# Kernel tuning notes

Hardware: AMD Instinct MI355X
Metric: run time of the kernel (lower is better)

Reference implementation:

```python
import jax, jax.numpy as jnp
import numpy as np

B, F_IN, N, S = 2, 128, 192, 192   # batch, in_features, n_nodes, seq (seq==n_nodes required by mask broadcast)
H, D = 4, 64                        # n_heads, n_hidden (out_features = H*D = 256)
NEG_SLOPE = 0.2


def setup_inputs() -> dict:
    key = jax.random.key(0)
    ks = jax.random.split(key, 6)
    X = jax.random.normal(ks[0], (B, F_IN, N, S), dtype=jnp.float32)
    A = jax.random.randint(ks[1], (N, N, 1), 0, 2, dtype=jnp.int32)
    W_lin = jax.random.normal(ks[2], (F_IN, H * D), dtype=jnp.float32) * 0.05
    b_lin = jax.random.uniform(ks[3], (H * D,), dtype=jnp.float32)
    W_attn = jax.random.normal(ks[4], (2 * D,), dtype=jnp.float32) * 0.05
    b_attn = jax.random.uniform(ks[5], (1,), dtype=jnp.float32)
    return {"X": X, "A": A, "W_lin": W_lin, "b_lin": b_lin,
            "W_attn": W_attn, "b_attn": b_attn}


def reference(X, A, W_lin, b_lin, W_attn, b_attn):
    # Dropout is identity (eval mode).
    b, f, n, s = X.shape
    x = jnp.transpose(X, (0, 3, 2, 1))                      # (b, s, n, f)
    g = (x @ W_lin + b_lin).reshape(b, s, n, H, D)          # (b, s, n, H, D)
    # attn is affine: attn(cat[g_i, g_j]) = a_src.g_i + a_dst.g_j + b_attn
    a_src, a_dst = W_attn[:D], W_attn[D:]
    s_src = jnp.einsum('bsnhd,d->bsnh', g, a_src)
    s_dst = jnp.einsum('bsnhd,d->bsnh', g, a_dst)
    e = s_src[:, :, :, None, :] + s_dst[:, :, None, :, :] + b_attn[0]  # (b, s, n_i, n_j, H)
    e = jnp.where(e >= 0, e, NEG_SLOPE * e)                 # LeakyReLU
    # torch masked_fill broadcast: mask (n,n,1,1) aligns with e dims (s, n_i, n_j, H)
    e = jnp.where(A[..., None] == 0, -jnp.inf, e)
    alphas = jax.nn.softmax(e, axis=1)                      # softmax over seq dim (dim=1, as in source)
    alphas = jnp.nan_to_num(alphas, nan=0.0)
    # einsum 'mnojh,klphf->mnohf': independent sums over j (alphas) and k,l,p (g)
    sum_g = g.sum(axis=(0, 1, 2))                           # (H, D)
    attn_res = alphas.sum(axis=3)[..., None] * sum_g        # (b, s, n, H, D)
    out = attn_res.reshape(b, s, n, H * D)                  # concat=True
    return jnp.transpose(out, (0, 3, 2, 1))                 # (b, out_features, n, s)
```

## Files before the change

### kernel.cpp

```cpp
#include <hip/hip_runtime.h>
#include <math.h>

#define B_ 2
#define F_ 128
#define N_ 192
#define S_ 192
#define NS_ (N_ * S_)
#define SLOPE 0.2f
#define LOG2E 1.4426950408889634f
#define NEG_INF (-__builtin_inff())

#if defined(__has_builtin)
#if __has_builtin(__builtin_amdgcn_exp2f)
#define EXP2(x) __builtin_amdgcn_exp2f(x)
#else
#define EXP2(x) exp2f(x)
#endif
#else
#define EXP2(x) exp2f(x)
#endif

__device__ __forceinline__ float lrelu(float e) { return fmaxf(e, SLOPE * e); }

#define OFF_WSRC 0
#define OFF_WDST 512
#define OFF_CSRC 1024
#define OFF_CDST 1028
#define OFF_SUMG 1040
#define OFF_PART 1296
#define OFF_SRC  2320
#define OFF_DST2 (OFF_SRC + 8 * NS_)
#define OFF_DST1 (OFF_DST2 + 8 * NS_)
#define OFF_ALPHA (OFF_DST1 + 8 * NS_)

__global__ __launch_bounds__(256) void kPre(const float* __restrict__ X,
                                            const float* __restrict__ W_lin,
                                            const float* __restrict__ b_lin,
                                            const float* __restrict__ W_attn,
                                            const float* __restrict__ b_attn,
                                            float* __restrict__ ws) {
    int blk = blockIdx.x, t = threadIdx.x;
    if (blk < 1024) {
        int sq = blk & 3, f = (blk >> 2) & 127, b = blk >> 9;
        const float4* p = (const float4*)(X + ((size_t)(b * F_ + f)) * NS_ + sq * 9216);
        float acc = 0.f;
#pragma unroll
        for (int k = 0; k < 9; k++) {
            float4 v = p[t + k * 256];
            acc += (v.x + v.y) + (v.z + v.w);
        }
        for (int o = 32; o; o >>= 1) acc += __shfl_down(acc, o, 64);
        __shared__ float red[4];
        if ((t & 63) == 0) red[t >> 6] = acc;
        __syncthreads();
        if (t == 0)
            ws[OFF_PART + sq * 256 + b * 128 + f] = (red[0] + red[1]) + (red[2] + red[3]);
    } else if (blk == 1024) {
        const float4* wa = (const float4*)W_attn;
        for (int c = t; c < 512; c += 256) {
            int f = c >> 2, h = c & 3;
            const float4* wl = (const float4*)(W_lin + f * 256 + h * 64);
            float as = 0.f, ad = 0.f;
#pragma unroll
            for (int q = 0; q < 16; q++) {
                float4 w = wl[q], a1 = wa[q], a2 = wa[16 + q];
                as += w.x * a1.x + w.y * a1.y + w.z * a1.z + w.w * a1.w;
                ad += w.x * a2.x + w.y * a2.y + w.z * a2.z + w.w * a2.w;
            }
            ws[OFF_WSRC + c] = as * LOG2E;
            ws[OFF_WDST + c] = ad * LOG2E;
        }
    } else {
        if (t < 4) {
            float c = 0.f;
            for (int d = 0; d < 64; d++) c += b_lin[t * 64 + d] * W_attn[d];
            ws[OFF_CSRC + t] = (c + b_attn[0]) * LOG2E;
        } else if (t < 8) {
            int h = t - 4;
            float c = 0.f;
            for (int d = 0; d < 64; d++) c += b_lin[h * 64 + d] * W_attn[64 + d];
            ws[OFF_CDST + h] = c * LOG2E;
        }
    }
}

__global__ __launch_bounds__(256) void kProj(const float* __restrict__ X,
                                             const int* __restrict__ A,
                                             const float* __restrict__ W_lin,
                                             const float* __restrict__ b_lin,
                                             float* __restrict__ ws) {
    __shared__ float4 wsl[128], wdl[128];
    __shared__ float red[4 * 64 * 9];
    __shared__ float xs[128];
    __shared__ float wbuf[4096];
    int t = threadIdx.x, blk = blockIdx.x;
    if (blk < 1152) {
        int n = blk % 192, bsc = blk / 192;
        int b = bsc / 3, sc = bsc % 3;
        if (t < 128) {
            wsl[t] = ((const float4*)(ws + OFF_WSRC))[t];
            wdl[t] = ((const float4*)(ws + OFF_WDST))[t];
        }
        __syncthreads();
        int fq = t >> 6, lane = t & 63;
        int s = sc * 64 + lane;
        float aS[4] = {0, 0, 0, 0}, aD[4] = {0, 0, 0, 0};
        const float* xp = X + (size_t)(b * F_) * NS_ + n * S_ + s;
        int f0 = fq * 32;
#pragma unroll 8
        for (int fi = 0; fi < 32; fi++) {
            float x = xp[(size_t)(f0 + fi) * NS_];
            float4 w1 = wsl[f0 + fi], w2 = wdl[f0 + fi];
            aS[0] += x * w1.x; aS[1] += x * w1.y; aS[2] += x * w1.z; aS[3] += x * w1.w;
            aD[0] += x * w2.x; aD[1] += x * w2.y; aD[2] += x * w2.z; aD[3] += x * w2.w;
        }
        float* rp = red + t * 9;
#pragma unroll
        for (int h = 0; h < 4; h++) { rp[h] = aS[h]; rp[4 + h] = aD[h]; }
        __syncthreads();
#pragma unroll
        for (int c = t; c < 512; c += 256) {
            int k = c >> 6, s_loc = c & 63;
            float v = red[s_loc * 9 + k] + red[(64 + s_loc) * 9 + k] +
                      red[(128 + s_loc) * 9 + k] + red[(192 + s_loc) * 9 + k];
            int ss = sc * 64 + s_loc;
            if (k < 4) {
                int bh = b * 4 + k;
                bool masked = (A[ss * 192 + n] == 0);
                ws[OFF_SRC + bh * NS_ + n * 192 + ss] =
                    masked ? NEG_INF : (v + ws[OFF_CSRC + k]);
            } else {
                int h = k - 4, bh = b * 4 + h;
                float dv = v + ws[OFF_CDST + h];
                ws[OFF_DST2 + bh * NS_ + n * 192 + ss] = dv;
                ws[OFF_DST1 + bh * NS_ + ss * 192 + n] = dv;
            }
        }
    } else {
        if (t < 128) {
            float v = 0.f;
#pragma unroll
            for (int q = 0; q < 8; q++) v += ws[OFF_PART + q * 128 + t];
            xs[t] = v;
        }
        float acc = 0.f;
        for (int ch = 0; ch < 8; ch++) {
            const float4* s4 = (const float4*)(W_lin + ch * 4096);
            __syncthreads();
#pragma unroll
            for (int k = 0; k < 4; k++) ((float4*)wbuf)[t + k * 256] = s4[t + k * 256];
            __syncthreads();
#pragma unroll
            for (int fi = 0; fi < 16; fi++) acc += xs[ch * 16 + fi] * wbuf[fi * 256 + t];
        }
        ws[OFF_SUMG + t] = acc + 73728.f * b_lin[t];
    }
}

__global__ __launch_bounds__(384) void kAlpha(float* __restrict__ ws) {
    int blk = blockIdx.x, t = threadIdx.x;
    int bh = blk & 7, iq = blk >> 3;
    __shared__ float p_sh[384];
    __shared__ float zpart[2 * 384];
    __shared__ float zr_sh[384];
    const float* src = ws + OFF_SRC + bh * NS_;
    const float* d1 = ws + OFF_DST1 + bh * NS_;
    const float* d2 = ws + OFF_DST2 + bh * NS_;
    p_sh[t] = src[iq * 384 + t];
    __syncthreads();

    {
        int sq = t / 192, j = t - sq * 192;
        float z0 = 0.f, z1 = 0.f;
        const float* d1p = d1 + j;
#pragma unroll 8
        for (int s = sq * 96; s < sq * 96 + 96; s++) {
            float q = d1p[s * 192];
            z0 += EXP2(lrelu(p_sh[s] + q));
            z1 += EXP2(lrelu(p_sh[192 + s] + q));
        }
        zpart[sq * 384 + j] = z0;
        zpart[sq * 384 + 192 + j] = z1;
    }
    __syncthreads();
    {
        float Z = zpart[t] + zpart[384 + t];
        zr_sh[t] = (Z != 0.f) ? (1.f / Z) : 0.f;
    }
    __syncthreads();

    {
        int i_loc = t / 192, s = t - i_loc * 192;
        float pv = p_sh[t];
        const float* zr = zr_sh + i_loc * 192;
        float acc = 0.f;
#pragma unroll 8
        for (int j = 0; j < 192; j++) {
            float q = d2[j * 192 + s];
            acc += EXP2(lrelu(pv + q)) * zr[j];
        }
        int i = iq * 2 + i_loc;
        ws[OFF_ALPHA + bh * NS_ + i * 192 + s] = acc;
    }
}

__global__ __launch_bounds__(256) void kOut(const float* __restrict__ ws,
                                            float* __restrict__ out) {
    __shared__ float sg[256];
    int t = threadIdx.x;
    sg[t] = ws[OFF_SUMG + t];
    __syncthreads();
    int v = blockIdx.x * 256 + t;
    int s4 = v % 48;
    int u = v / 48;
    int i = u % 192; u /= 192;
    int dq = u & 3;  u >>= 2;
    int h = u & 3;
    int b = u >> 2;
    int bh = (b << 2) | h;
    float4 al = *(const float4*)(ws + OFF_ALPHA + (bh * 192 + i) * 192 + s4 * 4);
    float* op = out + (((size_t)(b * 256 + h * 64 + dq * 16)) * 192 + i) * 192 + s4 * 4;
    const float* sgp = sg + h * 64 + dq * 16;
#pragma unroll
    for (int d = 0; d < 16; d++) {
        float g = sgp[d];
        float4 o = make_float4(al.x * g, al.y * g, al.z * g, al.w * g);
        *(float4*)(op + (size_t)d * NS_) = o;
    }
}

extern "C" void kernel_launch(void* const* d_in, const int* in_sizes, int n_in,
                              void* d_out, int out_size, void* d_ws, size_t ws_size,
                              hipStream_t stream) {
    const float* X      = (const float*)d_in[0];
    const int*   A      = (const int*)d_in[1];
    const float* W_lin  = (const float*)d_in[2];
    const float* b_lin  = (const float*)d_in[3];
    const float* W_attn = (const float*)d_in[4];
    const float* b_attn = (const float*)d_in[5];
    float* out = (float*)d_out;
    float* ws  = (float*)d_ws;

    kPre<<<1026, 256, 0, stream>>>(X, W_lin, b_lin, W_attn, b_attn, ws);
    kProj<<<1153, 256, 0, stream>>>(X, A, W_lin, b_lin, ws);
    kAlpha<<<768, 384, 0, stream>>>(ws);
    kOut<<<1152, 256, 0, stream>>>(ws, out);
}
```

Baseline: 156.2 us.

## Skip masked adjacency entries in alpha kernel via precomputed compacted index lists

Builds per-node lists of unmasked sequence indices from the adjacency matrix in the pre-kernel. The alpha kernel iterates only over those entries for both the normaliser and the output sums, and masked outputs are zeroed in kProj. Each block now handles four rows instead of two, which halves the grid. This removes about half of the exp work, since the mask is roughly half zeros. In exchange, the kernel adds a serial list-building block, indirect gather loads, divergent loop bounds and lower occupancy.

```diff
diff --git a/kernel.cpp b/kernel.cpp
--- a/kernel.cpp
+++ b/kernel.cpp
@@ -32,8 +32,11 @@
 #define OFF_DST2 (OFF_SRC + 8 * NS_)
 #define OFF_DST1 (OFF_DST2 + 8 * NS_)
 #define OFF_ALPHA (OFF_DST1 + 8 * NS_)
+#define OFF_CNT   (OFF_ALPHA + 8 * NS_)
+#define OFF_SLIST (OFF_CNT + 192)
 
 __global__ __launch_bounds__(256) void kPre(const float* __restrict__ X,
+                                            const int* __restrict__ A,
                                             const float* __restrict__ W_lin,
                                             const float* __restrict__ b_lin,
                                             const float* __restrict__ W_attn,
@@ -70,7 +73,7 @@
             ws[OFF_WSRC + c] = as * LOG2E;
             ws[OFF_WDST + c] = ad * LOG2E;
         }
-    } else {
+    } else if (blk == 1025) {
         if (t < 4) {
             float c = 0.f;
             for (int d = 0; d < 64; d++) c += b_lin[t * 64 + d] * W_attn[d];
@@ -80,6 +83,16 @@
             float c = 0.f;
             for (int d = 0; d < 64; d++) c += b_lin[h * 64 + d] * W_attn[64 + d];
             ws[OFF_CDST + h] = c * LOG2E;
+        }
+    } else {
+        if (t < 192) {
+            int* icnt = (int*)(ws + OFF_CNT);
+            int* isl = (int*)(ws + OFF_SLIST) + t * 192;
+            int cnt = 0;
+            for (int s = 0; s < 192; s++) {
+                if (A[s * 192 + t] != 0) isl[cnt++] = s;
+            }
+            icnt[t] = cnt;
         }
     }
 }
@@ -129,6 +142,7 @@
                 bool masked = (A[ss * 192 + n] == 0);
                 ws[OFF_SRC + bh * NS_ + n * 192 + ss] =
                     masked ? NEG_INF : (v + ws[OFF_CSRC + k]);
+                if (masked) ws[OFF_ALPHA + bh * NS_ + n * 192 + ss] = 0.f;
             } else {
                 int h = k - 4, bh = b * 4 + h;
                 float dv = v + ws[OFF_CDST + h];
@@ -160,47 +174,68 @@
 __global__ __launch_bounds__(384) void kAlpha(float* __restrict__ ws) {
     int blk = blockIdx.x, t = threadIdx.x;
     int bh = blk & 7, iq = blk >> 3;
-    __shared__ float p_sh[384];
-    __shared__ float zpart[2 * 384];
-    __shared__ float zr_sh[384];
+    __shared__ float p_sh[768];
+    __shared__ float zpart[1536];
+    __shared__ float zr_sh[768];
+    __shared__ int sl_sh[768];
+    __shared__ int cnt_sh[4];
     const float* src = ws + OFF_SRC + bh * NS_;
     const float* d1 = ws + OFF_DST1 + bh * NS_;
     const float* d2 = ws + OFF_DST2 + bh * NS_;
-    p_sh[t] = src[iq * 384 + t];
+    const int* icnt = (const int*)(ws + OFF_CNT);
+    const int* isl = (const int*)(ws + OFF_SLIST);
+    p_sh[t] = src[iq * 768 + t];
+    p_sh[t + 384] = src[iq * 768 + 384 + t];
+    sl_sh[t] = isl[iq * 768 + t];
+    sl_sh[t + 384] = isl[iq * 768 + 384 + t];
+    if (t < 4) cnt_sh[t] = icnt[iq * 4 + t];
     __syncthreads();
 
     {
         int sq = t / 192, j = t - sq * 192;
-        float z0 = 0.f, z1 = 0.f;
-        const float* d1p = d1 + j;
+        float z[4] = {0.f, 0.f, 0.f, 0.f};
+#pragma unroll
+        for (int il = 0; il < 4; il++) {
+            int cnt = cnt_sh[il];
+            const float* pr = p_sh + il * 192;
+            const int* sl = sl_sh + il * 192;
+            for (int k = sq; k < cnt; k += 2) {
+                int s = sl[k];
+                float q = d1[s * 192 + j];
+                z[il] += EXP2(lrelu(pr[s] + q));
+            }
+        }
+#pragma unroll
+        for (int il = 0; il < 4; il++) zpart[(sq * 4 + il) * 192 + j] = z[il];
+    }
+    __syncthreads();
+    for (int k = t; k < 768; k += 384) {
+        float Z = zpart[k] + zpart[768 + k];
+        zr_sh[k] = (Z != 0.f) ? (1.f / Z) : 0.f;
+    }
+    __syncthreads();
+
+    {
+        int c0 = cnt_sh[0], c1 = cnt_sh[1], c2 = cnt_sh[2], c3 = cnt_sh[3];
+        int tot = c0 + c1 + c2 + c3;
+        float* al = ws + OFF_ALPHA + bh * NS_ + iq * 768;
+        for (int pp = t; pp < tot; pp += 384) {
+            int il, off;
+            if (pp < c0) { il = 0; off = pp; }
+            else if (pp < c0 + c1) { il = 1; off = pp - c0; }
+            else if (pp < c0 + c1 + c2) { il = 2; off = pp - c0 - c1; }
+            else { il = 3; off = pp - c0 - c1 - c2; }
+            int s = sl_sh[il * 192 + off];
+            float pv = p_sh[il * 192 + s];
+            const float* zr = zr_sh + il * 192;
+            float acc = 0.f;
 #pragma unroll 8
-        for (int s = sq * 96; s < sq * 96 + 96; s++) {
-            float q = d1p[s * 192];
-            z0 += EXP2(lrelu(p_sh[s] + q));
-            z1 += EXP2(lrelu(p_sh[192 + s] + q));
-        }
-        zpart[sq * 384 + j] = z0;
-        zpart[sq * 384 + 192 + j] = z1;
-    }
-    __syncthreads();
-    {
-        float Z = zpart[t] + zpart[384 + t];
-        zr_sh[t] = (Z != 0.f) ? (1.f / Z) : 0.f;
-    }
-    __syncthreads();
-
-    {
-        int i_loc = t / 192, s = t - i_loc * 192;
-        float pv = p_sh[t];
-        const float* zr = zr_sh + i_loc * 192;
-        float acc = 0.f;
-#pragma unroll 8
-        for (int j = 0; j < 192; j++) {
-            float q = d2[j * 192 + s];
-            acc += EXP2(lrelu(pv + q)) * zr[j];
-        }
-        int i = iq * 2 + i_loc;
-        ws[OFF_ALPHA + bh * NS_ + i * 192 + s] = acc;
+            for (int j = 0; j < 192; j++) {
+                float q = d2[j * 192 + s];
+                acc += EXP2(lrelu(pv + q)) * zr[j];
+            }
+            al[il * 192 + s] = acc;
+        }
     }
 }
 
@@ -241,8 +276,8 @@
     float* out = (float*)d_out;
     float* ws  = (float*)d_ws;
 
-    kPre<<<1026, 256, 0, stream>>>(X, W_lin, b_lin, W_attn, b_attn, ws);
+    kPre<<<1027, 256, 0, stream>>>(X, A, W_lin, b_lin, W_attn, b_attn, ws);
     kProj<<<1153, 256, 0, stream>>>(X, A, W_lin, b_lin, ws);
-    kAlpha<<<768, 384, 0, stream>>>(ws);
+    kAlpha<<<384, 384, 0, stream>>>(ws);
     kOut<<<1152, 256, 0, stream>>>(ws, out);
 }
```

Measured after the change: 232.4 us. 48.8% more time.
